# Kernel optimization log

Measured on AMD Instinct MI355X. Metric: run time of the kernel, lower is better.

## Reference

```python
import jax, jax.numpy as jnp
import numpy as np

B, NAP, NUSER, F = 64, 128, 128, 10
HID = 100

def _glorot(key, fan_in, fan_out):
    std = jnp.sqrt(2.0 / (fan_in + fan_out)).astype(jnp.float32)
    return jax.random.normal(key, (fan_in, fan_out), dtype=jnp.float32) * std

def setup_inputs() -> dict:
    key = jax.random.key(0)
    k0, k1, k2, k3 = jax.random.split(key, 4)
    Ain = jax.random.normal(k0, (B, NAP, NUSER, F), dtype=jnp.float32)
    W0 = _glorot(k1, NUSER, HID); b0 = jnp.zeros((HID,), jnp.float32)
    W1 = _glorot(k2, HID, HID);   b1 = jnp.zeros((HID,), jnp.float32)
    W2 = _glorot(k3, HID, NAP * NUSER); b2 = jnpps = jnp.zeros((NAP * NUSER,), jnp.float32)
    return {"Ain": Ain, "W0": W0, "b0": b0, "W1": W1, "b1": b1, "W2": W2, "b2": b2}

def reference(Ain, W0, b0, W1, b1, W2, b2):
    Bn, Nap, Nuser, Fn = Ain.shape
    BF = Bn * Fn
    # xNN.call: [B,Nap,Nuser,F] -> [B,F,Nap,Nuser] -> [BF,Nap,Nuser]
    A = jnp.transpose(Ain, (0, 3, 1, 2)).reshape(BF, Nap, Nuser)
    xin = (1.0 / Nap) * jnp.ones_like(A)              # [BF,Nap,Nuser]
    # L = A^T A  (graph Laplacian surrogate), [BF,Nuser,Nuser]
    L = jnp.einsum('bki,bkj->bij', A, A)
    e, v = jnp.linalg.eigh(L)                         # e:[BF,Nuser] v:[BF,Nuser,Nuser]
    # MLP on eigenvalues: Nuser -> 100 -> 100 -> Nap*Nuser
    y = jax.nn.relu(e @ W0 + b0)
    y = jax.nn.relu(y @ W1 + b1)
    y = y @ W2 + b2                                   # [BF, Nap*Nuser]
    # Original flattens to K = BF*Nap with k = b*Nap + a, and tiles v so
    # v_tiled[k] = v[k % BF]. Reindex k = t*BF + m to avoid materializing the tile:
    # d2[t,m] = d[t*BF+m], x2[t,m] = x[t*BF+m], eigvecs used = v[m].
    d = y.reshape(BF * Nap, Nuser)
    x = xin.reshape(BF * Nap, Nuser)
    d2 = d.reshape(Nap, BF, Nuser)
    x2 = x.reshape(Nap, BF, Nuser)
    # v diag(d) v^T x  ==  v @ (d * (v^T x))   (fused spectral reconstruction)
    vtx = jnp.einsum('mij,tmi->tmj', v, x2)           # [Nap,BF,Nuser]
    out2 = jnp.einsum('mij,tmj->tmi', v, d2 * vtx)    # [Nap,BF,Nuser]
    out = out2.reshape(BF * Nap, Nuser).reshape(BF, Nap, Nuser)
    return jnp.exp(out)
```

## Files before the change

### kernel.cpp

```cpp
#include <hip/hip_runtime.h>
#include <hip/hip_fp16.h>

#define NSWEEP 12

static constexpr int F_  = 10;
static constexpr int BF  = 640;
static constexpr int HID = 100;
static constexpr float MU = 512.0f;

typedef float f32x2 __attribute__((ext_vector_type(2)));
__device__ __forceinline__ f32x2 pk_fma(f32x2 a, f32x2 b, f32x2 c) {
    return __builtin_elementwise_fma(a, b, c);
}

template<int CTRL>
__device__ __forceinline__ float dpp_add(float x) {
    int t = __builtin_amdgcn_update_dpp(0, __float_as_int(x), CTRL, 0xF, 0xF, false);
    return x + __int_as_float(t);
}
__device__ __forceinline__ float reduce8(float x) {
    x = dpp_add<0xB1>(x);
    x = dpp_add<0x4E>(x);
    x = dpp_add<0x141>(x);
    return x;
}
template<int MODE>
__device__ __forceinline__ int mv_i(int x) {
    if constexpr (MODE == 8)
        return __builtin_amdgcn_update_dpp(0, x, 0x128, 0xF, 0xF, false);
    else if constexpr (MODE == 16)
        return __builtin_amdgcn_ds_swizzle(x, 0x401F);
    else
        return __builtin_amdgcn_ds_swizzle(x, 0x601F);
}
template<int MODE>
__device__ __forceinline__ float mv_f(float x) {
    return __int_as_float(mv_i<MODE>(__float_as_int(x)));
}
template<int MODE>
__device__ __forceinline__ void mv_arr(f32x2 (&P)[8]) {
    #pragma unroll
    for (int e = 0; e < 8; ++e) {
        P[e].x = mv_f<MODE>(P[e].x);
        P[e].y = mv_f<MODE>(P[e].y);
    }
}

__device__ __forceinline__ float rcpf(float x) { return __builtin_amdgcn_rcpf(x); }
__device__ __forceinline__ float rsqf(float x) { return __builtin_amdgcn_rsqf(x); }

__device__ __forceinline__ float pdot(const f32x2 (&P)[8], const f32x2 (&Q)[8]) {
    f32x2 a0 = P[0] * Q[0], a1 = P[1] * Q[1], a2 = P[2] * Q[2], a3 = P[3] * Q[3];
    a0 = pk_fma(P[4], Q[4], a0);
    a1 = pk_fma(P[5], Q[5], a1);
    a2 = pk_fma(P[6], Q[6], a2);
    a3 = pk_fma(P[7], Q[7], a3);
    const f32x2 r = (a0 + a1) + (a2 + a3);
    return reduce8(r.x + r.y);
}

__device__ __forceinline__ void jrotL(f32x2 (&P)[8], f32x2 (&Q)[8],
                                      float& np, float& nq) {
    const float pq = pdot(P, Q);
    if (pq * pq > 1e-28f * np * nq) {
        const float tau = (nq - np) * 0.5f * rcpf(pq);
        const float r   = __builtin_amdgcn_sqrtf(fmaf(tau, tau, 1.f));
        const float t   = rcpf(tau + copysignf(r, tau));
        const float c   = rsqf(fmaf(t, t, 1.f));
        const float s   = t * c;
        const f32x2 cc = {c, c}, ms = {-s, -s}, ps = {s, s};
        #pragma unroll
        for (int e = 0; e < 8; ++e) {
            const f32x2 pe = P[e];
            P[e] = pk_fma(ms, Q[e], cc * pe);
            Q[e] = pk_fma(ps, pe, cc * Q[e]);
        }
        np = fmaf(-t, pq, np);
        nq = fmaf( t, pq, nq);
    }
}

template<int MODE>
__device__ __forceinline__ void jrotX(f32x2 (&P)[8], float& np, const bool isp) {
    f32x2 part[8];
    #pragma unroll
    for (int e = 0; e < 8; ++e) {
        part[e].x = mv_f<MODE>(P[e].x);
        part[e].y = mv_f<MODE>(P[e].y);
    }
    const float npart = mv_f<MODE>(np);
    const float pq  = pdot(P, part);
    const float app = isp ? np : npart;
    const float aqq = isp ? npart : np;
    if (pq * pq > 1e-28f * app * aqq) {
        const float tau = (aqq - app) * 0.5f * rcpf(pq);
        const float r   = __builtin_amdgcn_sqrtf(fmaf(tau, tau, 1.f));
        const float t   = rcpf(tau + copysignf(r, tau));
        const float c   = rsqf(fmaf(t, t, 1.f));
        const float s   = t * c;
        const float sg_ = isp ? -s : s;
        const f32x2 cc = {c, c}, ss = {sg_, sg_};
        #pragma unroll
        for (int e = 0; e < 8; ++e)
            P[e] = pk_fma(ss, part[e], cc * P[e]);
        np = fmaf(isp ? -t : t, pq, np);
    }
}

__global__ __launch_bounds__(512, 4)
void eig_kernel(const float* __restrict__ Ain,
                float* __restrict__ e_out,
                float* __restrict__ s_out,
                __half* __restrict__ V_out)
{
    __shared__ float SH[16 * 512];
    __shared__ int   exid[31][4];
    __shared__ float key[128], csum[128];
    __shared__ int   idxs[128], rankv[128];

    const int tid = threadIdx.x;
    const int g   = tid >> 5;
    const int l   = tid & 31;
    const int sg  = l >> 3;
    const int l7  = l & 7;
    const int e0  = l7 * 16;
    const int slw = sg * 32 + l7 * 4;
    const int m   = blockIdx.x;
    const int bb  = m / F_;
    const int ff  = m % F_;

    f32x2 T[8], Bc[8];
    float nT, nB;
    int idT = 8 * g + sg;
    int idB = idT + 4;

    float* const wr1   = (g > 0) ? &SH[(g - 1) * 512 + slw] : &SH[15 * 512 + slw];
    const int    wr1s  = (g > 0) ? (g - 1) : 30;
    const float* const rdT  = &SH[((g == 1) ? 15 : (g - 2)) * 512 + slw];
    const int    rdTs  = (g == 1) ? 30 : (g - 2);
    const int    sBw   = 30 - g;
    float* const wrB   = &SH[((sBw == 29) ? 15 : (sBw - 15)) * 512 + slw];
    const int    sBr   = 29 - g;
    const float* const rdB =
        &SH[((sBr == 29) ? 15 : ((sBr == 14) ? 14 : (sBr - 15))) * 512 + slw];

    #pragma unroll
    for (int e = 0; e < 8; ++e) {
        T[e].x  = (e0 + 2 * e == idT)     ? MU : 0.f;
        T[e].y  = (e0 + 2 * e + 1 == idT) ? MU : 0.f;
        Bc[e].x = (e0 + 2 * e == idB)     ? MU : 0.f;
        Bc[e].y = (e0 + 2 * e + 1 == idB) ? MU : 0.f;
    }

    {
        const float* Ab = Ain + (size_t)bb * 128 * 128 * F_ + ff;
        for (int c0 = 0; c0 < 128; c0 += 32) {
            for (int t = tid; t < 4096; t += 512)
                SH[t] = Ab[(size_t)((c0 + (t >> 7)) * 128 + (t & 127)) * F_];
            __syncthreads();
            for (int j = 0; j < 32; ++j) {
                const float at = SH[j * 128 + idT];
                const float ab = SH[j * 128 + idB];
                const f32x2 at2 = {at, at}, ab2 = {ab, ab};
                #pragma unroll
                for (int t = 0; t < 4; ++t) {
                    const float4 a = *(const float4*)&SH[j * 128 + e0 + 4 * t];
                    const f32x2 lo = {a.x, a.y}, hi = {a.z, a.w};
                    T[2*t]    = pk_fma(lo, at2, T[2*t]);
                    T[2*t+1]  = pk_fma(hi, at2, T[2*t+1]);
                    Bc[2*t]   = pk_fma(lo, ab2, Bc[2*t]);
                    Bc[2*t+1] = pk_fma(hi, ab2, Bc[2*t+1]);
                }
            }
            __syncthreads();
        }
    }

    nT = pdot(T, T);
    nB = pdot(Bc, Bc);

    for (int sw = 0; sw < NSWEEP; ++sw) {
        {
            const bool p1 = sg < (sg ^ 1), p2 = sg < (sg ^ 2), p3 = sg < (sg ^ 3);
            jrotX<8>(T, nT, p1);   jrotX<8>(Bc, nB, p1);
            jrotX<16>(T, nT, p2);  jrotX<16>(Bc, nB, p2);
            jrotX<24>(T, nT, p3);  jrotX<24>(Bc, nB, p3);
        }

        for (int br = 0; br < 31; ++br) {
            jrotL(T, Bc, nT, nB);
            mv_arr<8>(Bc);  nB = mv_f<8>(nB);  idB = mv_i<8>(idB);
            jrotL(T, Bc, nT, nB);
            mv_arr<24>(Bc); nB = mv_f<24>(nB); idB = mv_i<24>(idB);
            jrotL(T, Bc, nT, nB);
            mv_arr<8>(Bc);  nB = mv_f<8>(nB);  idB = mv_i<8>(idB);
            jrotL(T, Bc, nT, nB);

            {
                const f32x2* src = (g > 0) ? T : Bc;
                #pragma unroll
                for (int t = 0; t < 4; ++t)
                    *(float4*)(wr1 + t * 128) =
                        make_float4(src[2*t].x, src[2*t].y, src[2*t+1].x, src[2*t+1].y);
                if (l7 == 0) exid[wr1s][sg] = (g > 0) ? idT : idB;
            }
            __syncthreads();
            if (g >= 1) {
                #pragma unroll
                for (int t = 0; t < 4; ++t) {
                    const float4 v = *(const float4*)(rdT + t * 128);
                    T[2*t]   = f32x2{v.x, v.y};
                    T[2*t+1] = f32x2{v.z, v.w};
                }
                idT = exid[rdTs][sg];
            }
            __syncthreads();
            if (g > 0) {
                #pragma unroll
                for (int t = 0; t < 4; ++t)
                    *(float4*)(wrB + t * 128) =
                        make_float4(Bc[2*t].x, Bc[2*t].y, Bc[2*t+1].x, Bc[2*t+1].y);
                if (l7 == 0) exid[sBw][sg] = idB;
            }
            __syncthreads();
            {
                #pragma unroll
                for (int t = 0; t < 4; ++t) {
                    const float4 v = *(const float4*)(rdB + t * 128);
                    Bc[2*t]   = f32x2{v.x, v.y};
                    Bc[2*t+1] = f32x2{v.z, v.w};
                }
                idB = exid[sBr][sg];
            }
            __syncthreads();
            nT = pdot(T, T);
            nB = pdot(Bc, Bc);
        }
    }

    {
        float ca = 0.f, cb = 0.f;
        #pragma unroll
        for (int e = 0; e < 8; ++e) {
            ca += T[e].x + T[e].y;
            cb += Bc[e].x + Bc[e].y;
        }
        const float a = pdot(T, T);
        const float b = pdot(Bc, Bc);
        ca = reduce8(ca); cb = reduce8(cb);
        const float ivT = 1.f / sqrtf(a);
        const float ivB = 1.f / sqrtf(b);
        if (l7 == 0) {
            key[idT] = a;  csum[idT] = ca * ivT * (1.f / 128.f);
            key[idB] = b;  csum[idB] = cb * ivB * (1.f / 128.f);
        }
        __syncthreads();
        if (tid < 128) idxs[tid] = tid;
        __syncthreads();
        for (int kk = 2; kk <= 128; kk <<= 1) {
            for (int jj = kk >> 1; jj > 0; jj >>= 1) {
                if (tid < 128) {
                    const int i = tid, l2 = i ^ jj;
                    if (l2 > i) {
                        const bool up = ((i & kk) == 0);
                        const float ki = key[i], kl = key[l2];
                        if ((ki > kl) == up) {
                            const int ii = idxs[i], il = idxs[l2];
                            key[i] = kl; key[l2] = ki;
                            idxs[i] = il; idxs[l2] = ii;
                        }
                    }
                }
                __syncthreads();
            }
        }
        if (tid < 128) rankv[idxs[tid]] = tid;
        __syncthreads();
        if (tid < 128) {
            e_out[(size_t)m * 128 + tid] = sqrtf(key[tid]) - MU;
            s_out[(size_t)m * 128 + tid] = csum[idxs[tid]];
        }
        __half* Vb = V_out + (size_t)m * 16384;
        const int rkT = rankv[idT], rkB = rankv[idB];
        unsigned int wT[8], wB[8];
        #pragma unroll
        for (int t = 0; t < 8; ++t) {
            __half2 hT = __floats2half2_rn(T[t].x * ivT,  T[t].y * ivT);
            __half2 hB = __floats2half2_rn(Bc[t].x * ivB, Bc[t].y * ivB);
            wT[t] = *(unsigned int*)&hT;
            wB[t] = *(unsigned int*)&hB;
        }
        *(uint4*)(Vb + rkT * 128 + e0)     = make_uint4(wT[0], wT[1], wT[2], wT[3]);
        *(uint4*)(Vb + rkT * 128 + e0 + 8) = make_uint4(wT[4], wT[5], wT[6], wT[7]);
        *(uint4*)(Vb + rkB * 128 + e0)     = make_uint4(wB[0], wB[1], wB[2], wB[3]);
        *(uint4*)(Vb + rkB * 128 + e0 + 8) = make_uint4(wB[4], wB[5], wB[6], wB[7]);
    }
}

__global__ __launch_bounds__(128)
void mlp_kernel(const float* __restrict__ e_in,
                const float* __restrict__ W0,
                const float* __restrict__ b0,
                const float* __restrict__ W1,
                const float* __restrict__ b1,
                float* __restrict__ y_out)
{
    __shared__ float ein[128];
    __shared__ float h0[HID];
    const int m = blockIdx.x;
    const int tid = threadIdx.x;
    ein[tid] = e_in[(size_t)m * 128 + tid];
    __syncthreads();
    if (tid < HID) {
        float a = b0[tid];
        for (int i = 0; i < 128; ++i) a += ein[i] * W0[i * HID + tid];
        h0[tid] = fmaxf(a, 0.f);
    }
    __syncthreads();
    if (tid < HID) {
        float a = b1[tid];
        for (int h = 0; h < HID; ++h) a += h0[h] * W1[h * HID + tid];
        y_out[(size_t)m * HID + tid] = fmaxf(a, 0.f);
    }
}

__global__ __launch_bounds__(256)
void final_kernel(const float* __restrict__ y,
                  const float* __restrict__ W2,
                  const float* __restrict__ b2,
                  const float* __restrict__ s_in,
                  const __half* __restrict__ V_in,
                  float* __restrict__ outp)
{
    extern __shared__ float lds[];
    float* Vs  = lds;
    float* Wm  = lds + 16512;
    float* Ys  = lds;
    float* W2s = lds + 12928;

    const int m    = blockIdx.x;
    const int m_hi = m >> 7, m_lo = m & 127;
    const int tid  = threadIdx.x;
    const int tx   = tid & 15, ty = tid >> 4;

    for (int u = tid; u < 128 * 100; u += 256) {
        const int t = u / 100, h = u - t * 100;
        Ys[t * 101 + h] = y[(size_t)(5 * t + m_hi) * 100 + h];
    }
    for (int u = tid; u < 100 * 128; u += 256) {
        const int h = u >> 7, c = u & 127;
        W2s[h * 128 + c] = W2[(size_t)h * 16384 + (size_t)m_lo * 128 + c];
    }
    __syncthreads();

    float acc[8][8];
    #pragma unroll
    for (int a = 0; a < 8; ++a)
        #pragma unroll
        for (int c = 0; c < 8; ++c) acc[a][c] = 0.f;
    for (int h = 0; h < 100; ++h) {
        float yv[8], wv[8];
        #pragma unroll
        for (int a = 0; a < 8; ++a) yv[a] = Ys[(ty + 16 * a) * 101 + h];
        #pragma unroll
        for (int c = 0; c < 8; ++c) wv[c] = W2s[h * 128 + tx + 16 * c];
        #pragma unroll
        for (int a = 0; a < 8; ++a)
            #pragma unroll
            for (int c = 0; c < 8; ++c) acc[a][c] += yv[a] * wv[c];
    }
    {
        float b2v[8], sv[8];
        #pragma unroll
        for (int c = 0; c < 8; ++c) {
            b2v[c] = b2[m_lo * 128 + tx + 16 * c];
            sv[c]  = s_in[(size_t)m * 128 + tx + 16 * c];
        }
        #pragma unroll
        for (int a = 0; a < 8; ++a)
            #pragma unroll
            for (int c = 0; c < 8; ++c)
                acc[a][c] = (acc[a][c] + b2v[c]) * sv[c];
    }
    __syncthreads();

    #pragma unroll
    for (int a = 0; a < 8; ++a)
        #pragma unroll
        for (int c = 0; c < 8; ++c)
            Wm[(ty + 16 * a) * 129 + tx + 16 * c] = acc[a][c];
    for (int u = tid; u < 16384; u += 256) {
        const int colj = u >> 7, k = u & 127;
        Vs[k * 129 + colj] = __half2float(V_in[(size_t)m * 16384 + u]);
    }
    __syncthreads();

    float o[8][8];
    #pragma unroll
    for (int a = 0; a < 8; ++a)
        #pragma unroll
        for (int c = 0; c < 8; ++c) o[a][c] = 0.f;
    for (int j = 0; j < 128; ++j) {
        float wv[8], vv[8];
        #pragma unroll
        for (int a = 0; a < 8; ++a) wv[a] = Wm[(ty + 16 * a) * 129 + j];
        #pragma unroll
        for (int c = 0; c < 8; ++c) vv[c] = Vs[(tx + 16 * c) * 129 + j];
        #pragma unroll
        for (int a = 0; a < 8; ++a)
            #pragma unroll
            for (int c = 0; c < 8; ++c) o[a][c] += wv[a] * vv[c];
    }
    #pragma unroll
    for (int a = 0; a < 8; ++a) {
        const int t = ty + 16 * a;
        const size_t rowbase = (size_t)(5 * t + m_hi) * 16384 + (size_t)m_lo * 128;
        #pragma unroll
        for (int c = 0; c < 8; ++c)
            outp[rowbase + tx + 16 * c] = expf(o[a][c]);
    }
}

extern "C" void kernel_launch(void* const* d_in, const int* in_sizes, int n_in,
                              void* d_out, int out_size, void* d_ws, size_t ws_size,
                              hipStream_t stream)
{
    const float* Ain = (const float*)d_in[0];
    const float* W0  = (const float*)d_in[1];
    const float* b0  = (const float*)d_in[2];
    const float* W1  = (const float*)d_in[3];
    const float* b1  = (const float*)d_in[4];
    const float* W2  = (const float*)d_in[5];
    const float* b2  = (const float*)d_in[6];
    float* outp = (float*)d_out;

    char* ws = (char*)d_ws;
    __half* Vh  = (__half*)ws;
    float* e_ws = (float*)(ws + 20971520);
    float* s_ws = (float*)(ws + 20971520 + 327680);
    float* y_ws = (float*)(ws + 20971520 + 655360);

    const size_t lds_bytes = (size_t)(2 * 128 * 129) * sizeof(float);

    eig_kernel<<<dim3(BF), dim3(512), 0, stream>>>(Ain, e_ws, s_ws, Vh);
    mlp_kernel<<<dim3(BF), dim3(128), 0, stream>>>(e_ws, W0, b0, W1, b1, y_ws);
    final_kernel<<<dim3(BF), dim3(256), lds_bytes, stream>>>(y_ws, W2, b2, s_ws, Vh, outp);
}
```

Before: 2.292 ms.

## Use intra-wavefront bpermute for column rotation exchange, halving block barriers

The round-robin Jacobi column exchange between the 32-lane groups now handles pairs that share a 64-lane wavefront through ds_bpermute (lane xor 32), without going through shared memory. Only cross-wavefront handoffs are written to LDS, and they are all done in one write/read phase. This cuts the __syncthreads count per rotation step from four to two and shrinks the shared buffers. In exchange there are extra bpermute ops, more register pressure from the Y temporaries, and a more intricate ordering mapping that has to stay correct.

```diff
diff --git a/kernel.cpp b/kernel.cpp
--- a/kernel.cpp
+++ b/kernel.cpp
@@ -113,8 +113,8 @@
                 float* __restrict__ s_out,
                 __half* __restrict__ V_out)
 {
-    __shared__ float SH[16 * 512];
-    __shared__ int   exid[31][4];
+    __shared__ float SH[14 * 512];
+    __shared__ int   exid[14][4];
     __shared__ float key[128], csum[128];
     __shared__ int   idxs[128], rankv[128];
 
@@ -125,6 +125,7 @@
     const int l7  = l & 7;
     const int e0  = l7 * 16;
     const int slw = sg * 32 + l7 * 4;
+    const int bpa = (((tid & 63) ^ 32) << 2);
     const int m   = blockIdx.x;
     const int bb  = m / F_;
     const int ff  = m % F_;
@@ -134,15 +135,18 @@
     int idT = 8 * g + sg;
     int idB = idT + 4;
 
-    float* const wr1   = (g > 0) ? &SH[(g - 1) * 512 + slw] : &SH[15 * 512 + slw];
-    const int    wr1s  = (g > 0) ? (g - 1) : 30;
-    const float* const rdT  = &SH[((g == 1) ? 15 : (g - 2)) * 512 + slw];
-    const int    rdTs  = (g == 1) ? 30 : (g - 2);
-    const int    sBw   = 30 - g;
-    float* const wrB   = &SH[((sBw == 29) ? 15 : (sBw - 15)) * 512 + slw];
-    const int    sBr   = 29 - g;
-    const float* const rdB =
-        &SH[((sBr == 29) ? 15 : ((sBr == 14) ? 14 : (sBr - 15))) * 512 + slw];
+    const bool low  = ((g & 1) == 0);
+    const bool pw_t = (!low) && (g <= 13);
+    const bool pr_t = low && (g >= 2);
+    const bool pw_b = low && (g >= 2);
+    const bool pr_b = (!low) && (g <= 13);
+    float* const wrT = &SH[(g >> 1) * 512 + slw];
+    const float* const rdT = &SH[((g - 1) >> 1) * 512 + slw];
+    float* const wrB = &SH[(6 + (g >> 1)) * 512 + slw];
+    const float* const rdB = &SH[(6 + ((g + 1) >> 1)) * 512 + slw];
+    const int wrTs = g >> 1, rdTs = (g - 1) >> 1;
+    const int wrBs = 6 + (g >> 1), rdBs = 6 + ((g + 1) >> 1);
+    const bool blendT = low && (g != 0);
 
     #pragma unroll
     for (int e = 0; e < 8; ++e) {
@@ -195,17 +199,35 @@
             jrotL(T, Bc, nT, nB);
             mv_arr<8>(Bc);  nB = mv_f<8>(nB);  idB = mv_i<8>(idB);
             jrotL(T, Bc, nT, nB);
-
-            {
-                const f32x2* src = (g > 0) ? T : Bc;
+            mv_arr<24>(Bc); nB = mv_f<24>(nB); idB = mv_i<24>(idB);
+
+            f32x2 Y[8];
+            int yid;
+            #pragma unroll
+            for (int e = 0; e < 8; ++e) {
+                const float xx = blendT ? T[e].x : Bc[e].x;
+                const float xy = blendT ? T[e].y : Bc[e].y;
+                Y[e].x = __int_as_float(__builtin_amdgcn_ds_bpermute(bpa, __float_as_int(xx)));
+                Y[e].y = __int_as_float(__builtin_amdgcn_ds_bpermute(bpa, __float_as_int(xy)));
+            }
+            yid = __builtin_amdgcn_ds_bpermute(bpa, blendT ? idT : idB);
+
+            if (pw_t) {
                 #pragma unroll
                 for (int t = 0; t < 4; ++t)
-                    *(float4*)(wr1 + t * 128) =
-                        make_float4(src[2*t].x, src[2*t].y, src[2*t+1].x, src[2*t+1].y);
-                if (l7 == 0) exid[wr1s][sg] = (g > 0) ? idT : idB;
+                    *(float4*)(wrT + t * 128) =
+                        make_float4(T[2*t].x, T[2*t].y, T[2*t+1].x, T[2*t+1].y);
+                if (l7 == 0) exid[wrTs][sg] = idT;
+            }
+            if (pw_b) {
+                #pragma unroll
+                for (int t = 0; t < 4; ++t)
+                    *(float4*)(wrB + t * 128) =
+                        make_float4(Bc[2*t].x, Bc[2*t].y, Bc[2*t+1].x, Bc[2*t+1].y);
+                if (l7 == 0) exid[wrBs][sg] = idB;
             }
             __syncthreads();
-            if (g >= 1) {
+            if (pr_t) {
                 #pragma unroll
                 for (int t = 0; t < 4; ++t) {
                     const float4 v = *(const float4*)(rdT + t * 128);
@@ -214,25 +236,32 @@
                 }
                 idT = exid[rdTs][sg];
             }
-            __syncthreads();
-            if (g > 0) {
-                #pragma unroll
-                for (int t = 0; t < 4; ++t)
-                    *(float4*)(wrB + t * 128) =
-                        make_float4(Bc[2*t].x, Bc[2*t].y, Bc[2*t+1].x, Bc[2*t+1].y);
-                if (l7 == 0) exid[sBw][sg] = idB;
-            }
-            __syncthreads();
-            {
+            if (pr_b) {
                 #pragma unroll
                 for (int t = 0; t < 4; ++t) {
                     const float4 v = *(const float4*)(rdB + t * 128);
                     Bc[2*t]   = f32x2{v.x, v.y};
                     Bc[2*t+1] = f32x2{v.z, v.w};
                 }
-                idB = exid[sBr][sg];
+                idB = exid[rdBs][sg];
             }
             __syncthreads();
+
+            if (g == 15) {
+                #pragma unroll
+                for (int e = 0; e < 8; ++e) Bc[e] = T[e];
+                idB = idT;
+            }
+            if (!low) {
+                #pragma unroll
+                for (int e = 0; e < 8; ++e) T[e] = Y[e];
+                idT = yid;
+            } else {
+                #pragma unroll
+                for (int e = 0; e < 8; ++e) Bc[e] = Y[e];
+                idB = yid;
+            }
+
             nT = pdot(T, T);
             nB = pdot(Bc, Bc);
         }
```

Result: slower. 2.402 ms (+4.8%).
